# Optimization experiments

Measured on AMD Instinct MI355X. Metric: run time of the kernel, lower is better.

## Reference

```python
import jax, jax.numpy as jnp
import numpy as np

V, EMB, H, N, E, B = 100000, 300, 64, 20000, 160000, 4096
L, T = 2, 3  # layer_timesteps = [3, 3]


def setup_inputs() -> dict:
    key = jax.random.key(0)
    ks = jax.random.split(key, 24)
    ri = lambda k, shape, hi: jax.random.randint(k, shape, 0, hi)
    rn = lambda k, shape, s=0.05: (jax.random.normal(k, shape, dtype=jnp.float32) * s)
    emb_table = rn(ks[7], (V, EMB), 0.1).at[0].set(0.0)  # padding_idx=0 row is zeros
    return {
        'emb_ind0': ri(ks[0], (N,), V),
        'emb_ind1': ri(ks[1], (N,), V),
        'adj0': ri(ks[2], (E, 2), N),
        'adj1': ri(ks[3], (E, 2), N),
        'prop_ind0': ri(ks[4], (B,), N),
        'prop_ind1': ri(ks[5], (B,), N),
        'labels': ri(ks[6], (B,), 2),
        'emb_table': emb_table,
        'proj_W': rn(ks[8], (EMB, H)),   # emb_proj weight (stored input-major)
        'proj_b': jnp.zeros((H,), jnp.float32),
        'msg_W': rn(ks[9], (L, H, H)),   # per-layer edge-type-0 message linear
        'msg_b': jnp.zeros((L, H), jnp.float32),
        'gru_Wih': rn(ks[10], (L, 3 * H, H)),
        'gru_Whh': rn(ks[11], (L, 3 * H, H)),
        'gru_bih': jnp.zeros((L, 3 * H), jnp.float32),
        'gru_bhh': jnp.zeros((L, 3 * H), jnp.float32),
        'cla_W1': rn(ks[12], (2 * H, 16)),
        'cla_b1': jnp.zeros((16,), jnp.float32),
        'cla_W2': rn(ks[13], (16, 1)),
        'cla_b2': jnp.zeros((1,), jnp.float32),
    }


def _gru_cell(x, h, Wih, Whh, bih, bhh):
    # torch.nn.GRUCell math
    gi = x @ Wih.T + bih
    gh = h @ Whh.T + bhh
    i_r, i_z, i_n = jnp.split(gi, 3, axis=-1)
    h_r, h_z, h_n = jnp.split(gh, 3, axis=-1)
    r = jax.nn.sigmoid(i_r + h_r)
    z = jax.nn.sigmoid(i_z + h_z)
    n = jnp.tanh(i_n + r * h_n)
    return (1.0 - z) * n + z * h


def reference(emb_ind0, emb_ind1, adj0, adj1, prop_ind0, prop_ind1, labels,
              emb_table, proj_W, proj_b, msg_W, msg_b,
              gru_Wih, gru_Whh, gru_bih, gru_bhh,
              cla_W1, cla_b1, cla_W2, cla_b2):
    def ggnn(x, adj):
        src, tgt = adj[:, 0], adj[:, 1]
        h = x
        for l in range(L):              # 2 structurally distinct layers
            for _ in range(T):          # 3 timesteps each
                m = h[src] @ msg_W[l] + msg_b[l]                     # [E, H] gather + transform
                inc = jax.ops.segment_sum(m, tgt, num_segments=N)    # scatter-add messages
                h = _gru_cell(inc, h, gru_Wih[l], gru_Whh[l], gru_bih[l], gru_bhh[l])
        return h

    def branch(emb_ind, adj, prop_ind):
        ge = emb_table[emb_ind]          # embedding lookup [N, EMB]
        ge = ge @ proj_W + proj_b        # emb_proj -> [N, H]
        ge = ggnn(ge, adj)
        return ge[prop_ind]              # index_select -> [B, H]

    g0 = branch(emb_ind0, adj0, prop_ind0)
    g1 = branch(emb_ind1, adj1, prop_ind1)
    ge = jnp.concatenate([g0, g1], axis=-1)                 # match='concat' -> [B, 2H]
    hid = jax.nn.relu(ge @ cla_W1 + cla_b1)
    logits = jax.nn.sigmoid(hid @ cla_W2 + cla_b2)          # [B, 1], num_class=1 path
    p = logits.squeeze(-1)
    y = labels.astype(p.dtype)
    eps = 1e-7  # mirrors torch BCELoss log-clamping
    loss = -jnp.mean(y * jnp.log(jnp.clip(p, eps, 1.0))
                     + (1.0 - y) * jnp.log(jnp.clip(1.0 - p, eps, 1.0)))
    return logits, loss
```

## Files before the change

kernel.cpp:

```cpp
#include <hip/hip_runtime.h>
#include <hip/hip_bf16.h>

typedef unsigned short u16;
typedef __attribute__((ext_vector_type(8))) short s16x8;
typedef __attribute__((ext_vector_type(4))) float f32x4;

#define NN 20000
#define HH 64
#define EMBD 300
#define EE 160000
#define BB 4096
#define NODES 40000

#define OFF_PROJB 0
#define OFF_MSGB  64
#define OFF_BIH   192
#define OFF_BHH   576
#define OFF_CW1T  960
#define OFF_CB1   3008
#define OFF_CW2   3024
#define OFF_CB2   3040
#define PARAM_SZ  3072

#define PB_WIH   0
#define PB_WHH   24576
#define PB_WMT   49152
#define PB_PROJT 57344
#define PB_SZ    77824

#define APAD 344

#define ZCNT (16 + 2 * (NN + 1))

__device__ __forceinline__ float b2f(u16 u) {
    union { unsigned int i; float f; } v; v.i = ((unsigned int)u) << 16; return v.f;
}
__device__ __forceinline__ u16 f2b(float f) {
    union { float f; unsigned int u; } v; v.f = f;
    unsigned int u = v.u;
    return (u16)((u + 0x7FFFu + ((u >> 16) & 1u)) >> 16);
}
__device__ __forceinline__ float ldf(const void* p, long long i, int isbf) {
    return isbf ? b2f(((const u16*)p)[i]) : ((const float*)p)[i];
}
__device__ __forceinline__ u16 ldb(const void* p, long long i, int isbf) {
    return isbf ? ((const u16*)p)[i] : f2b(((const float*)p)[i]);
}
__device__ __forceinline__ void stf(void* p, long long i, int isbf, float v) {
    if (isbf) ((u16*)p)[i] = f2b(v);
    else      ((float*)p)[i] = v;
}

__device__ __forceinline__ int sniff_inline(const u16* probe, int tid)
{
    u16 x = probe[2 * (tid & 63)];
    unsigned int e = (x >> 7) & 0xFF;
    unsigned long long m = __ballot(e >= 105 && e <= 127);
    return (__popcll(m) >= 48) ? 1 : 0;
}

__global__ __launch_bounds__(256) void conv_kernel(
    const void* projW, const void* projb, const void* msgW, const void* msgb,
    const void* wih, const void* whh, const void* bih, const void* bhh,
    const void* cw1, const void* cb1, const void* cw2, const void* cb2,
    float* P, u16* PB, int* zbase)
{
    int tid = threadIdx.x;
    int isbf = sniff_inline((const u16*)projW, tid);
    int i = blockIdx.x * 256 + tid;

    if (i < ZCNT) zbase[i] = 0;

    if (i < 64)    P[OFF_PROJB + i] = ldf(projb, i, isbf);
    if (i < 128)   P[OFF_MSGB + i]  = ldf(msgb, i, isbf);
    if (i < 384)   { P[OFF_BIH + i] = ldf(bih, i, isbf); P[OFF_BHH + i] = ldf(bhh, i, isbf); }
    if (i < 2048)  { int t = i >> 7, k = i & 127; P[OFF_CW1T + i] = ldf(cw1, (long long)k * 16 + t, isbf); }
    if (i < 16)    { P[OFF_CB1 + i] = ldf(cb1, i, isbf); P[OFF_CW2 + i] = ldf(cw2, i, isbf); }
    if (i == 0)    P[OFF_CB2] = ldf(cb2, 0, isbf);

    if (i < 24576) {
        int l = i / 12288, r = i - l * 12288;
        int frag = r >> 9, rr = r & 511, lane = rr >> 3, e = rr & 7;
        int jt = frag >> 1, kt = frag & 1;
        int srow = jt * 16 + (lane & 15);
        int sk = kt * 32 + ((lane >> 4) << 3) + e;
        long long si = (long long)l * 12288 + srow * 64 + sk;
        PB[PB_WIH + i] = ldb(wih, si, isbf);
        PB[PB_WHH + i] = ldb(whh, si, isbf);
    }
    if (i < 8192) {
        int l = i >> 12, r = i & 4095;
        int frag = r >> 9, rr = r & 511, lane = rr >> 3, e = rr & 7;
        int jt = frag >> 1, kt = frag & 1;
        int srow = jt * 16 + (lane & 15);
        int sk = kt * 32 + ((lane >> 4) << 3) + e;
        PB[PB_WMT + i] = ldb(msgW, (long long)l * 4096 + sk * 64 + srow, isbf);
    }
    if (i < 20480) {
        int frag = i >> 9, rr = i & 511, lane = rr >> 3, e = rr & 7;
        int jt = frag / 10, kt = frag - jt * 10;
        int srow = jt * 16 + (lane & 15);
        int sk = kt * 32 + ((lane >> 4) << 3) + e;
        PB[PB_PROJT + i] = (sk < 300) ? ldb(projW, (long long)sk * 64 + srow, isbf) : (u16)0;
    }
}

__global__ __launch_bounds__(256) void hist_kernel(const int* __restrict__ adj0,
                                                   const int* __restrict__ adj1, int* off)
{
    int e = blockIdx.x * 256 + threadIdx.x;
    if (e >= 2 * EE) return;
    int b = e / EE, le = e - b * EE;
    const int* adj = b ? adj1 : adj0;
    int tgt = adj[2 * le + 1];
    atomicAdd(&off[b * (NN + 1) + tgt + 1], 1);
}

__global__ __launch_bounds__(1024) void scan_kernel(int* off, int* cursor)
{
    int b = blockIdx.x;
    int* o = off + (size_t)b * (NN + 1);
    int* cur = cursor + (size_t)b * NN;
    __shared__ int wsum[16];
    __shared__ int woff_s[16];
    int tid = threadIdx.x, wv = tid >> 6, lane = tid & 63;

    int base = tid * 20;
    int v[20];
    int tot = 0;
    #pragma unroll
    for (int k = 0; k < 20; ++k) {
        int i = base + k;
        int x = (i < NN) ? o[i + 1] : 0;
        tot += x;
        v[k] = tot;
    }
    int incl = tot;
    #pragma unroll
    for (int d = 1; d < 64; d <<= 1) {
        int t = __shfl_up(incl, d);
        if (lane >= d) incl += t;
    }
    if (lane == 63) wsum[wv] = incl;
    int lane_excl = incl - tot;
    __syncthreads();
    if (tid < 16) {
        int w = wsum[tid];
        int s = w;
        #pragma unroll
        for (int d = 1; d < 16; d <<= 1) {
            int t = __shfl_up(s, d, 16);
            if (tid >= d) s += t;
        }
        woff_s[tid] = s - w;
    }
    __syncthreads();
    int pexcl = woff_s[wv] + lane_excl;
    int run = pexcl;
    #pragma unroll
    for (int k = 0; k < 20; ++k) {
        int i = base + k;
        if (i < NN) { o[i] = run; cur[i] = run; }
        run = pexcl + v[k];
    }
    if (tid == 1023) o[NN] = pexcl;
}

__global__ __launch_bounds__(256) void scatter_kernel(const int* __restrict__ adj0,
                                                      const int* __restrict__ adj1,
                                                      int* cursor, int* esrc)
{
    int e = blockIdx.x * 256 + threadIdx.x;
    if (e >= 2 * EE) return;
    int b = e / EE, le = e - b * EE;
    const int* adj = b ? adj1 : adj0;
    int src = adj[2 * le + 0];
    int tgt = adj[2 * le + 1];
    int pos = atomicAdd(&cursor[b * NN + tgt], 1);
    esrc[(size_t)b * EE + pos] = src;
}

__global__ __launch_bounds__(256) void projm_kernel(const void* emb,
                                                    const int* __restrict__ i0,
                                                    const int* __restrict__ i1,
                                                    const float* __restrict__ P,
                                                    const u16* __restrict__ PB,
                                                    u16* __restrict__ h,
                                                    const u16* __restrict__ probe)
{
    __shared__ u16 sA[64 * APAD];
    int tid = threadIdx.x;
    int isbf = sniff_inline(probe, tid);
    int node0 = blockIdx.x * 64;
    int wv = tid >> 6, lane = tid & 63;

    {
        int oct = lane & 7;
        int rbase = wv * 16 + (lane >> 3);
        #pragma unroll
        for (int rr = 0; rr < 2; ++rr) {
            int r = rbase + rr * 8;
            int n = node0 + r;
            int bb2 = n >= NN;
            int ln = n - bb2 * NN;
            int idx = bb2 ? i1[ln] : i0[ln];
            u16* dst = sA + r * APAD;
            if (isbf) {
                const u16* src = (const u16*)emb + (size_t)idx * EMBD;
                if ((idx & 1) == 0) {
                    for (int c = oct; c < 37; c += 8)
                        *(uint4*)(dst + c * 8) = *(const uint4*)(src + c * 8);
                    if (oct == 7)
                        *(uint2*)(dst + 296) = *(const uint2*)(src + 296);
                } else {
                    for (int c = oct; c < 75; c += 8)
                        *(uint2*)(dst + c * 4) = *(const uint2*)(src + c * 4);
                }
                if (oct == 0) {
                    ushort4 z = {0, 0, 0, 0};
                    ushort4* d4 = (ushort4*)dst;
                    #pragma unroll
                    for (int c = 75; c < 80; ++c) d4[c] = z;
                }
            } else {
                const float4* src = (const float4*)((const float*)emb + (size_t)idx * EMBD);
                for (int c = oct; c < 75; c += 8) {
                    float4 f = src[c];
                    ushort4 o4 = { f2b(f.x), f2b(f.y), f2b(f.z), f2b(f.w) };
                    *(ushort4*)(dst + c * 4) = o4;
                }
                if (oct == 0) {
                    ushort4 z = {0, 0, 0, 0};
                    ushort4* d4 = (ushort4*)dst;
                    #pragma unroll
                    for (int c = 75; c < 80; ++c) d4[c] = z;
                }
            }
        }
    }

    int quad = lane >> 4, cn = lane & 15;
    int m0 = wv * 16;
    f32x4 acc[4];
    #pragma unroll
    for (int j = 0; j < 4; ++j) {
        float bb = P[OFF_PROJB + j * 16 + cn];
        acc[j] = {bb, bb, bb, bb};
    }
    #pragma unroll
    for (int kt = 0; kt < 10; ++kt) {
        s16x8 a = *(const s16x8*)&sA[(m0 + cn) * APAD + kt * 32 + quad * 8];
        #pragma unroll
        for (int j = 0; j < 4; ++j) {
            s16x8 bfr = *(const s16x8*)&PB[PB_PROJT + (j * 10 + kt) * 512 + lane * 8];
            acc[j] = __builtin_amdgcn_mfma_f32_16x16x32_bf16(a, bfr, acc[j], 0, 0, 0);
        }
    }
    #pragma unroll
    for (int j = 0; j < 4; ++j)
        #pragma unroll
        for (int r = 0; r < 4; ++r)
            h[(size_t)(node0 + m0 + quad * 4 + r) * 64 + j * 16 + cn] = f2b(acc[j][r]);
}

__global__ __launch_bounds__(256) void fstep_kernel(const u16* __restrict__ h_old,
                                                    u16* __restrict__ h_new,
                                                    const int* __restrict__ ioff,
                                                    const int* __restrict__ esrc,
                                                    const float* __restrict__ P,
                                                    const u16* __restrict__ PB, int l)
{
    __shared__ u16 s_S[32 * 64];
    __shared__ u16 s_h[32 * 64];
    __shared__ u16 s_inc[32 * 64];
    __shared__ float s_deg[32];

    int tid = threadIdx.x;
    int bsw = blockIdx.x;
    int half = (bsw >> 2) & 1;
    int t = (bsw >> 3) * 4 + (bsw & 3);
    if (t >= 625) return;
    int node0 = half * NN + t * 32;

    {
        int team = tid >> 3, oct = tid & 7;
        int node = node0 + team;
        int br = node >= NN;
        int ln = node - br * NN;
        const int* o = ioff + (size_t)br * (NN + 1);
        int s0 = o[ln], s1 = o[ln + 1];
        const int* es = esrc + (size_t)br * EE;
        const u16* hb = h_old + (size_t)br * NN * 64;

        *(uint4*)&s_h[team * 64 + oct * 8] =
            *(const uint4*)&h_old[(size_t)node * 64 + oct * 8];
        if (oct == 0) s_deg[team] = (float)(s1 - s0);

        float acc[8];
        #pragma unroll
        for (int k = 0; k < 8; ++k) acc[k] = 0.f;

        int base = s0, rem = s1 - s0;
        while (rem > 0) {
            int cnt = rem < 8 ? rem : 8;
            int myidx = es[base + (oct < cnt ? oct : cnt - 1)];
            #pragma unroll
            for (int j = 0; j < 8; ++j) {
                int e = __shfl(myidx, j, 8);
                uint4 v = *(const uint4*)&hb[(size_t)e * 64 + oct * 8];
                float w = (j < cnt) ? 1.f : 0.f;
                #pragma unroll
                for (int p = 0; p < 4; ++p) {
                    unsigned int u = ((const unsigned int*)&v)[p];
                    union { unsigned int i; float f; } lo, hi;
                    lo.i = u << 16; hi.i = u & 0xffff0000u;
                    acc[2 * p]     += w * lo.f;
                    acc[2 * p + 1] += w * hi.f;
                }
            }
            base += cnt;
            rem -= cnt;
        }

        u16 pk[8];
        #pragma unroll
        for (int k = 0; k < 8; ++k) pk[k] = f2b(acc[k]);
        *(uint4*)&s_S[team * 64 + oct * 8] = *(const uint4*)pk;
    }
    __syncthreads();

    int wv = tid >> 6, lane = tid & 63;
    int wr = wv >> 1, wc = wv & 1;
    int m0 = wr * 16;
    int quad = lane >> 4, cn = lane & 15;
    int arow = (m0 + cn) * 64 + quad * 8;
    int fl = lane * 8;

    s16x8 aS0 = *(const s16x8*)&s_S[arow];
    s16x8 aS1 = *(const s16x8*)&s_S[arow + 32];
    s16x8 aH0 = *(const s16x8*)&s_h[arow];
    s16x8 aH1 = *(const s16x8*)&s_h[arow + 32];

    const u16* WM = PB + PB_WMT + (size_t)l * 4096;
    #pragma unroll
    for (int jtl = 0; jtl < 2; ++jtl) {
        int jt = wc * 2 + jtl;
        float mb = P[OFF_MSGB + l * 64 + jt * 16 + cn];
        f32x4 acc;
        acc[0] = s_deg[m0 + quad * 4 + 0] * mb;
        acc[1] = s_deg[m0 + quad * 4 + 1] * mb;
        acc[2] = s_deg[m0 + quad * 4 + 2] * mb;
        acc[3] = s_deg[m0 + quad * 4 + 3] * mb;
        acc = __builtin_amdgcn_mfma_f32_16x16x32_bf16(aS0, *(const s16x8*)&WM[(jt * 2 + 0) * 512 + fl], acc, 0, 0, 0);
        acc = __builtin_amdgcn_mfma_f32_16x16x32_bf16(aS1, *(const s16x8*)&WM[(jt * 2 + 1) * 512 + fl], acc, 0, 0, 0);
        #pragma unroll
        for (int r = 0; r < 4; ++r)
            s_inc[(m0 + quad * 4 + r) * 64 + jt * 16 + cn] = f2b(acc[r]);
    }
    __syncthreads();

    s16x8 aI0 = *(const s16x8*)&s_inc[arow];
    s16x8 aI1 = *(const s16x8*)&s_inc[arow + 32];
    const u16* WI = PB + PB_WIH + (size_t)l * 12288;
    const u16* WH = PB + PB_WHH + (size_t)l * 12288;
    const float* bi = P + OFF_BIH + l * 192;
    const float* bh = P + OFF_BHH + l * 192;

    #pragma unroll
    for (int cl = 0; cl < 2; ++cl) {
        int jt = wc * 2 + cl;
        int j0 = jt * 16;
        float vr = bi[j0 + cn], vz = bi[64 + j0 + cn], vn = bi[128 + j0 + cn];
        float wr_ = bh[j0 + cn], wz = bh[64 + j0 + cn], wn = bh[128 + j0 + cn];
        f32x4 gr = {vr, vr, vr, vr}, gz = {vz, vz, vz, vz}, gn = {vn, vn, vn, vn};
        f32x4 hr = {wr_, wr_, wr_, wr_}, hz = {wz, wz, wz, wz}, hn = {wn, wn, wn, wn};
        int fr = (jt * 2) * 512 + fl, frz = ((4 + jt) * 2) * 512 + fl, frn = ((8 + jt) * 2) * 512 + fl;
        gr = __builtin_amdgcn_mfma_f32_16x16x32_bf16(aI0, *(const s16x8*)&WI[fr], gr, 0, 0, 0);
        gr = __builtin_amdgcn_mfma_f32_16x16x32_bf16(aI1, *(const s16x8*)&WI[fr + 512], gr, 0, 0, 0);
        gz = __builtin_amdgcn_mfma_f32_16x16x32_bf16(aI0, *(const s16x8*)&WI[frz], gz, 0, 0, 0);
        gz = __builtin_amdgcn_mfma_f32_16x16x32_bf16(aI1, *(const s16x8*)&WI[frz + 512], gz, 0, 0, 0);
        gn = __builtin_amdgcn_mfma_f32_16x16x32_bf16(aI0, *(const s16x8*)&WI[frn], gn, 0, 0, 0);
        gn = __builtin_amdgcn_mfma_f32_16x16x32_bf16(aI1, *(const s16x8*)&WI[frn + 512], gn, 0, 0, 0);
        hr = __builtin_amdgcn_mfma_f32_16x16x32_bf16(aH0, *(const s16x8*)&WH[fr], hr, 0, 0, 0);
        hr = __builtin_amdgcn_mfma_f32_16x16x32_bf16(aH1, *(const s16x8*)&WH[fr + 512], hr, 0, 0, 0);
        hz = __builtin_amdgcn_mfma_f32_16x16x32_bf16(aH0, *(const s16x8*)&WH[frz], hz, 0, 0, 0);
        hz = __builtin_amdgcn_mfma_f32_16x16x32_bf16(aH1, *(const s16x8*)&WH[frz + 512], hz, 0, 0, 0);
        hn = __builtin_amdgcn_mfma_f32_16x16x32_bf16(aH0, *(const s16x8*)&WH[frn], hn, 0, 0, 0);
        hn = __builtin_amdgcn_mfma_f32_16x16x32_bf16(aH1, *(const s16x8*)&WH[frn + 512], hn, 0, 0, 0);
        #pragma unroll
        for (int r = 0; r < 4; ++r) {
            int row = m0 + quad * 4 + r;
            float rr = 1.f / (1.f + __expf(-(gr[r] + hr[r])));
            float zz = 1.f / (1.f + __expf(-(gz[r] + hz[r])));
            float nn = tanhf(gn[r] + rr * hn[r]);
            float ho = b2f(s_h[row * 64 + j0 + cn]);
            s_S[row * 64 + j0 + cn] = f2b((1.f - zz) * nn + zz * ho);
        }
    }
    __syncthreads();

    {
        int team = tid >> 3, oct = tid & 7;
        int node = node0 + team;
        *(uint4*)&h_new[(size_t)node * 64 + oct * 8] =
            *(const uint4*)&s_S[team * 64 + oct * 8];
    }
}

__global__ __launch_bounds__(256) void cls_kernel(const u16* __restrict__ h,
                                                  const int* __restrict__ p0,
                                                  const int* __restrict__ p1,
                                                  const int* __restrict__ labels,
                                                  const float* __restrict__ P,
                                                  void* out, float* partial,
                                                  const u16* __restrict__ probe)
{
    int tid = threadIdx.x;
    int isbf = sniff_inline(probe, tid);
    int wv = tid >> 6, lane = tid & 63;
    int s = blockIdx.x * 4 + wv;
    int n0 = p0[s], n1 = p1[s];
    float f0 = b2f(h[(size_t)n0 * 64 + lane]);
    float f1 = b2f(h[(size_t)(NN + n1) * 64 + lane]);
    float z = P[OFF_CB2];
    #pragma unroll
    for (int t = 0; t < 16; ++t) {
        float part = f0 * P[OFF_CW1T + t * 128 + lane] + f1 * P[OFF_CW1T + t * 128 + 64 + lane];
        #pragma unroll
        for (int off = 32; off; off >>= 1) part += __shfl_xor(part, off);
        z += fmaxf(part + P[OFF_CB1 + t], 0.f) * P[OFF_CW2 + t];
    }
    float p = 1.f / (1.f + expf(-z));
    float y = (float)labels[s];
    const float eps = 1e-7f;
    float pc  = fminf(fmaxf(p, eps), 1.f);
    float pc1 = fminf(fmaxf(1.f - p, eps), 1.f);
    float term = y * logf(pc) + (1.f - y) * logf(pc1);
    __shared__ float red[4];
    if (lane == 0) { stf(out, s, isbf, p); red[wv] = term; }
    __syncthreads();
    if (tid == 0) partial[blockIdx.x] = red[0] + red[1] + red[2] + red[3];
}

__global__ __launch_bounds__(256) void loss_kernel(const float* __restrict__ partial,
                                                   void* out, const u16* __restrict__ probe)
{
    int tid = threadIdx.x;
    int isbf = sniff_inline(probe, tid);
    __shared__ float red[256];
    float s = 0.f;
    for (int i = tid; i < 1024; i += 256) s += partial[i];
    red[tid] = s;
    __syncthreads();
    for (int d = 128; d > 0; d >>= 1) {
        if (tid < d) red[tid] += red[tid + d];
        __syncthreads();
    }
    if (tid == 0) stf(out, BB, isbf, -red[0] / (float)BB);
}

extern "C" void kernel_launch(void* const* d_in, const int* in_sizes, int n_in,
                              void* d_out, int out_size, void* d_ws, size_t ws_size,
                              hipStream_t stream)
{
    const int* adj0   = (const int*)d_in[2];
    const int* adj1   = (const int*)d_in[3];
    const int* prop0  = (const int*)d_in[4];
    const int* prop1  = (const int*)d_in[5];
    const int* labels = (const int*)d_in[6];
    const u16* probe  = (const u16*)d_in[8];

    float* P  = (float*)d_ws + 16;
    u16* PB   = (u16*)(P + PARAM_SZ);
    u16* h0   = (u16*)(((uintptr_t)(PB + PB_SZ) + 255) & ~(uintptr_t)255);
    u16* h1   = h0 + (size_t)NODES * 64;
    float* partial = (float*)(h1 + (size_t)NODES * 64);
    int* zbase  = (int*)(partial + 1024);
    int* ioff   = zbase + 16;
    int* cursor = ioff + 2 * (NN + 1) + 62;
    int* esrc   = cursor + 2 * NN;

    conv_kernel<<<157, 256, 0, stream>>>(d_in[8], d_in[9], d_in[10], d_in[11], d_in[12], d_in[13],
                                         d_in[14], d_in[15], d_in[16], d_in[17], d_in[18], d_in[19],
                                         P, PB, zbase);
    hist_kernel<<<(2 * EE) / 256, 256, 0, stream>>>(adj0, adj1, ioff);
    scan_kernel<<<2, 1024, 0, stream>>>(ioff, cursor);
    scatter_kernel<<<(2 * EE) / 256, 256, 0, stream>>>(adj0, adj1, cursor, esrc);
    projm_kernel<<<(2 * NN) / 64, 256, 0, stream>>>(d_in[7], (const int*)d_in[0],
                                                    (const int*)d_in[1], P, PB, h0, probe);

    u16* hcur = h0;
    u16* hnext = h1;
    for (int l = 0; l < 2; ++l) {
        for (int t = 0; t < 3; ++t) {
            fstep_kernel<<<1256, 256, 0, stream>>>(hcur, hnext, ioff, esrc, P, PB, l);
            u16* tmp = hcur; hcur = hnext; hnext = tmp;
        }
    }

    cls_kernel<<<BB / 4, 256, 0, stream>>>(hcur, prop0, prop1, labels, P, d_out,
                                           partial, probe);
    loss_kernel<<<1, 256, 0, stream>>>(partial, d_out, probe);
}
```

Baseline: 386.3 us.

## Halve nodes per fused step block, use 16 lanes per node gather

The fused GGNN step kernel now handles 16 nodes per 256-thread block instead of 32. Each node is gathered by a 16-lane team loading 8-byte chunks, and each wave computes one 16-column tile rather than two. The grid doubles to 2504 blocks, and launch bounds request 6 blocks per SM, to expose more parallelism for the latency-bound gather over 40000 nodes. In exchange, the per-block weight-fragment loads and synchronisation are amortised over fewer nodes, and the narrower 8-byte gather loads may use memory transactions less efficiently.

```diff
diff --git a/kernel.cpp b/kernel.cpp
--- a/kernel.cpp
+++ b/kernel.cpp
@@ -263,27 +263,27 @@
             h[(size_t)(node0 + m0 + quad * 4 + r) * 64 + j * 16 + cn] = f2b(acc[j][r]);
 }
 
-__global__ __launch_bounds__(256) void fstep_kernel(const u16* __restrict__ h_old,
-                                                    u16* __restrict__ h_new,
-                                                    const int* __restrict__ ioff,
-                                                    const int* __restrict__ esrc,
-                                                    const float* __restrict__ P,
-                                                    const u16* __restrict__ PB, int l)
-{
-    __shared__ u16 s_S[32 * 64];
-    __shared__ u16 s_h[32 * 64];
-    __shared__ u16 s_inc[32 * 64];
-    __shared__ float s_deg[32];
+__global__ __launch_bounds__(256, 6) void fstep_kernel(const u16* __restrict__ h_old,
+                                                       u16* __restrict__ h_new,
+                                                       const int* __restrict__ ioff,
+                                                       const int* __restrict__ esrc,
+                                                       const float* __restrict__ P,
+                                                       const u16* __restrict__ PB, int l)
+{
+    __shared__ u16 s_S[16 * 64];
+    __shared__ u16 s_h[16 * 64];
+    __shared__ u16 s_inc[16 * 64];
+    __shared__ float s_deg[16];
 
     int tid = threadIdx.x;
     int bsw = blockIdx.x;
     int half = (bsw >> 2) & 1;
     int t = (bsw >> 3) * 4 + (bsw & 3);
-    if (t >= 625) return;
-    int node0 = half * NN + t * 32;
+    if (t >= 1250) return;
+    int node0 = half * NN + t * 16;
 
     {
-        int team = tid >> 3, oct = tid & 7;
+        int team = tid >> 4, oct = tid & 15;
         int node = node0 + team;
         int br = node >= NN;
         int ln = node - br * NN;
@@ -292,26 +292,26 @@
         const int* es = esrc + (size_t)br * EE;
         const u16* hb = h_old + (size_t)br * NN * 64;
 
-        *(uint4*)&s_h[team * 64 + oct * 8] =
-            *(const uint4*)&h_old[(size_t)node * 64 + oct * 8];
+        *(uint2*)&s_h[team * 64 + oct * 4] =
+            *(const uint2*)&h_old[(size_t)node * 64 + oct * 4];
         if (oct == 0) s_deg[team] = (float)(s1 - s0);
 
-        float acc[8];
-        #pragma unroll
-        for (int k = 0; k < 8; ++k) acc[k] = 0.f;
+        float acc[4];
+        #pragma unroll
+        for (int k = 0; k < 4; ++k) acc[k] = 0.f;
 
         int base = s0, rem = s1 - s0;
         while (rem > 0) {
-            int cnt = rem < 8 ? rem : 8;
+            int cnt = rem < 16 ? rem : 16;
             int myidx = es[base + (oct < cnt ? oct : cnt - 1)];
             #pragma unroll
-            for (int j = 0; j < 8; ++j) {
-                int e = __shfl(myidx, j, 8);
-                uint4 v = *(const uint4*)&hb[(size_t)e * 64 + oct * 8];
+            for (int j = 0; j < 16; ++j) {
+                int e = __shfl(myidx, j, 16);
+                uint2 v = *(const uint2*)&hb[(size_t)e * 64 + oct * 4];
                 float w = (j < cnt) ? 1.f : 0.f;
                 #pragma unroll
-                for (int p = 0; p < 4; ++p) {
-                    unsigned int u = ((const unsigned int*)&v)[p];
+                for (int p = 0; p < 2; ++p) {
+                    unsigned int u = (p == 0) ? v.x : v.y;
                     union { unsigned int i; float f; } lo, hi;
                     lo.i = u << 16; hi.i = u & 0xffff0000u;
                     acc[2 * p]     += w * lo.f;
@@ -322,18 +322,17 @@
             rem -= cnt;
         }
 
-        u16 pk[8];
-        #pragma unroll
-        for (int k = 0; k < 8; ++k) pk[k] = f2b(acc[k]);
-        *(uint4*)&s_S[team * 64 + oct * 8] = *(const uint4*)pk;
+        u16 pk[4];
+        #pragma unroll
+        for (int k = 0; k < 4; ++k) pk[k] = f2b(acc[k]);
+        *(uint2*)&s_S[team * 64 + oct * 4] = *(const uint2*)pk;
     }
     __syncthreads();
 
     int wv = tid >> 6, lane = tid & 63;
-    int wr = wv >> 1, wc = wv & 1;
-    int m0 = wr * 16;
+    int jt = wv;
     int quad = lane >> 4, cn = lane & 15;
-    int arow = (m0 + cn) * 64 + quad * 8;
+    int arow = cn * 64 + quad * 8;
     int fl = lane * 8;
 
     s16x8 aS0 = *(const s16x8*)&s_S[arow];
@@ -342,20 +341,18 @@
     s16x8 aH1 = *(const s16x8*)&s_h[arow + 32];
 
     const u16* WM = PB + PB_WMT + (size_t)l * 4096;
-    #pragma unroll
-    for (int jtl = 0; jtl < 2; ++jtl) {
-        int jt = wc * 2 + jtl;
+    {
         float mb = P[OFF_MSGB + l * 64 + jt * 16 + cn];
         f32x4 acc;
-        acc[0] = s_deg[m0 + quad * 4 + 0] * mb;
-        acc[1] = s_deg[m0 + quad * 4 + 1] * mb;
-        acc[2] = s_deg[m0 + quad * 4 + 2] * mb;
-        acc[3] = s_deg[m0 + quad * 4 + 3] * mb;
+        acc[0] = s_deg[quad * 4 + 0] * mb;
+        acc[1] = s_deg[quad * 4 + 1] * mb;
+        acc[2] = s_deg[quad * 4 + 2] * mb;
+        acc[3] = s_deg[quad * 4 + 3] * mb;
         acc = __builtin_amdgcn_mfma_f32_16x16x32_bf16(aS0, *(const s16x8*)&WM[(jt * 2 + 0) * 512 + fl], acc, 0, 0, 0);
         acc = __builtin_amdgcn_mfma_f32_16x16x32_bf16(aS1, *(const s16x8*)&WM[(jt * 2 + 1) * 512 + fl], acc, 0, 0, 0);
         #pragma unroll
         for (int r = 0; r < 4; ++r)
-            s_inc[(m0 + quad * 4 + r) * 64 + jt * 16 + cn] = f2b(acc[r]);
+            s_inc[(quad * 4 + r) * 64 + jt * 16 + cn] = f2b(acc[r]);
     }
     __syncthreads();
 
@@ -366,9 +363,7 @@
     const float* bi = P + OFF_BIH + l * 192;
     const float* bh = P + OFF_BHH + l * 192;
 
-    #pragma unroll
-    for (int cl = 0; cl < 2; ++cl) {
-        int jt = wc * 2 + cl;
+    {
         int j0 = jt * 16;
         float vr = bi[j0 + cn], vz = bi[64 + j0 + cn], vn = bi[128 + j0 + cn];
         float wr_ = bh[j0 + cn], wz = bh[64 + j0 + cn], wn = bh[128 + j0 + cn];
@@ -389,7 +384,7 @@
         hn = __builtin_amdgcn_mfma_f32_16x16x32_bf16(aH1, *(const s16x8*)&WH[frn + 512], hn, 0, 0, 0);
         #pragma unroll
         for (int r = 0; r < 4; ++r) {
-            int row = m0 + quad * 4 + r;
+            int row = quad * 4 + r;
             float rr = 1.f / (1.f + __expf(-(gr[r] + hr[r])));
             float zz = 1.f / (1.f + __expf(-(gz[r] + hz[r])));
             float nn = tanhf(gn[r] + rr * hn[r]);
@@ -400,10 +395,10 @@
     __syncthreads();
 
     {
-        int team = tid >> 3, oct = tid & 7;
+        int team = tid >> 4, oct = tid & 15;
         int node = node0 + team;
-        *(uint4*)&h_new[(size_t)node * 64 + oct * 8] =
-            *(const uint4*)&s_S[team * 64 + oct * 8];
+        *(uint2*)&h_new[(size_t)node * 64 + oct * 4] =
+            *(const uint2*)&s_S[team * 64 + oct * 4];
     }
 }
 
@@ -493,7 +488,7 @@
     u16* hnext = h1;
     for (int l = 0; l < 2; ++l) {
         for (int t = 0; t < 3; ++t) {
-            fstep_kernel<<<1256, 256, 0, stream>>>(hcur, hnext, ioff, esrc, P, PB, l);
+            fstep_kernel<<<2504, 256, 0, stream>>>(hcur, hnext, ioff, esrc, P, PB, l);
             u16* tmp = hcur; hcur = hnext; hnext = tmp;
         }
     }
```

Result: no change. 380.2 us (-1.6%).
